# Kernel optimization log

Measured on AMD Instinct MI355X. Metric: run time of the kernel, lower is better.

The kernel has to match this reference:

```python
import jax, jax.numpy as jnp
import numpy as np

B, S, H = 4, 2048, 1024
E, K = 8, 2

def setup_inputs() -> dict:
    key = jax.random.key(0)
    ks = jax.random.split(key, 5)
    scale = 1.0 / np.sqrt(H)
    return {
        "x": jax.random.normal(ks[0], (B, S, H), dtype=jnp.float32),
        "router_w": jax.random.uniform(ks[1], (E, H), jnp.float32, -scale, scale),
        "router_b": jax.random.uniform(ks[2], (E,), jnp.float32, -scale, scale),
        "expert_w": jax.random.uniform(ks[3], (E, H, H), jnp.float32, -scale, scale),
        "expert_b": jax.random.uniform(ks[4], (E, H), jnp.float32, -scale, scale),
    }


def reference(x, router_w, router_b, expert_w, expert_b):
    # Router: [b,s,E]
    scores = jnp.einsum("bsh,eh->bse", x, router_w) + router_b
    probs = jax.nn.softmax(scores, axis=-1)
    p, expert_id = jax.lax.top_k(probs, K)          # [b,s,K]
    # Renormalize top-k probs (matches p / p.sum(dim=2))
    p = p / jnp.sum(p, axis=-1, keepdims=True)
    # Per-token combine weight per expert: [b,s,E]
    onehot = jax.nn.one_hot(expert_id, E, dtype=x.dtype)  # [b,s,K,E]
    w_comb = jnp.einsum("bske,bsk->bse", onehot, p)
    # All-expert linear (Linear: x @ W.T + b): [b,s,E,h]
    all_out = jnp.einsum("bsh,edh->bsed", x, expert_w) + expert_b
    # Weighted combine over selected experts: [b,s,h]
    return jnp.einsum("bse,bsed->bsd", w_comb, all_out)
```

## Files before the change

### kernel.cpp

```cpp
#include <hip/hip_runtime.h>
#include <hip/hip_bf16.h>
#include <math.h>

#define TOK 8192
#define HD 1024
#define NE 8
#define SLOTS 17408

typedef _Float16 half8 __attribute__((ext_vector_type(8)));
typedef _Float16 half4v __attribute__((ext_vector_type(4)));
typedef float floatx4 __attribute__((ext_vector_type(4)));

__global__ void moe_score(const float* __restrict__ x,
                          const float* __restrict__ rw,
                          const float* __restrict__ rb,
                          int* __restrict__ epair,
                          float* __restrict__ w1out,
                          _Float16* __restrict__ xh) {
  const int lane = threadIdx.x & 63;
  const int wid = threadIdx.x >> 6;
  const int t = blockIdx.x * 4 + wid;
  const float4* xp = (const float4*)(x + (size_t)t * HD);
  float4 xr[4];
#pragma unroll
  for (int i = 0; i < 4; ++i) xr[i] = xp[lane + 64 * i];
  if (xh) {
    _Float16* xo = xh + (size_t)t * HD;
#pragma unroll
    for (int i = 0; i < 4; ++i) {
      half4v h = {(_Float16)xr[i].x, (_Float16)xr[i].y,
                  (_Float16)xr[i].z, (_Float16)xr[i].w};
      *(half4v*)(xo + (lane + 64 * i) * 4) = h;
    }
  }
  float sc[NE];
#pragma unroll
  for (int e = 0; e < NE; ++e) {
    const float4* wp = (const float4*)(rw + e * HD);
    float a = 0.f;
#pragma unroll
    for (int i = 0; i < 4; ++i) {
      float4 w = wp[lane + 64 * i];
      a += xr[i].x * w.x + xr[i].y * w.y + xr[i].z * w.z + xr[i].w * w.w;
    }
#pragma unroll
    for (int off = 32; off > 0; off >>= 1) a += __shfl_xor(a, off);
    sc[e] = a + rb[e];
  }
  float b1 = sc[0]; int e1 = 0;
#pragma unroll
  for (int e = 1; e < NE; ++e) if (sc[e] > b1) { b1 = sc[e]; e1 = e; }
  float b2 = -1e30f; int e2 = 0;
#pragma unroll
  for (int e = 0; e < NE; ++e) { if (e != e1 && sc[e] > b2) { b2 = sc[e]; e2 = e; } }
  if (lane == 0) {
    epair[t] = e1 | (e2 << 8);
    w1out[t] = 1.f / (1.f + expf(b2 - b1));
  }
}

__global__ void moe_count(const int* __restrict__ epair, int* __restrict__ cntp) {
  __shared__ int lc[NE];
  const int tid = threadIdx.x;
  if (tid < NE) lc[tid] = 0;
  __syncthreads();
  int ep = epair[blockIdx.x * 256 + tid];
  atomicAdd(&lc[ep & 0xff], 1);
  atomicAdd(&lc[ep >> 8], 1);
  __syncthreads();
  if (tid < NE) atomicAdd(&cntp[tid * 64], lc[tid]);
}

__global__ void moe_prefix(const int* __restrict__ cntp, int* __restrict__ cnt2,
                           int* __restrict__ base) {
  if (threadIdx.x == 0) {
    int b = 0;
    for (int e = 0; e < NE; ++e) {
      base[e] = b;
      cnt2[e * 64] = b;
      b += (cntp[e * 64] + 127) & ~127;
    }
  }
}

__global__ void moe_scatter(const int* __restrict__ epair,
                            const float* __restrict__ w1in,
                            int* __restrict__ cnt2,
                            int* __restrict__ tok_list,
                            float* __restrict__ tok_w,
                            int* __restrict__ slot_of) {
  __shared__ int lcnt[NE];
  __shared__ int lbase[NE];
  const int tid = threadIdx.x;
  const int t = blockIdx.x * 256 + tid;
  if (tid < NE) lcnt[tid] = 0;
  __syncthreads();
  int ep = epair[t];
  int e1 = ep & 0xff, e2 = ep >> 8;
  float w1 = w1in[t];
  int o1 = atomicAdd(&lcnt[e1], 1);
  int o2 = atomicAdd(&lcnt[e2], 1);
  __syncthreads();
  if (tid < NE) lbase[tid] = atomicAdd(&cnt2[tid * 64], lcnt[tid]);
  __syncthreads();
  int s1 = lbase[e1] + o1;
  tok_list[s1] = t; tok_w[s1] = w1; slot_of[2 * t] = s1;
  int s2 = lbase[e2] + o2;
  tok_list[s2] = t; tok_w[s2] = 1.f - w1; slot_of[2 * t + 1] = s2;
}

__global__ void cvt_f32_f16(const float* __restrict__ src,
                            _Float16* __restrict__ dst, int n4) {
  int i = blockIdx.x * 256 + threadIdx.x;
  if (i >= n4) return;
  float4 v = ((const float4*)src)[i];
  half4v h = {(_Float16)v.x, (_Float16)v.y, (_Float16)v.z, (_Float16)v.w};
  ((half4v*)dst)[i] = h;
}

template <int EPI>
__global__ __launch_bounds__(256) void moe_gemm(
    const _Float16* __restrict__ Ah, const _Float16* __restrict__ Bh,
    const float* __restrict__ eb,
    const int* __restrict__ cntp, const int* __restrict__ base,
    const int* __restrict__ tok_list, const float* __restrict__ tok_w,
    _Float16* __restrict__ scratch, float* __restrict__ out) {
  const int e = blockIdx.z;
  const int ce = cntp[e * 64];
  const int m0 = blockIdx.y * 128;
  if (m0 >= ce) return;
  const int sbase = base[e];
  const int n0 = blockIdx.x * 128;
  const int tid = threadIdx.x;
  const int lane = tid & 63;
  const int wid = tid >> 6;
  const int wm = wid & 1, wn = wid >> 1;

  __shared__ _Float16 A_s[128 * 64];
  __shared__ _Float16 B_s[128 * 64];
  __shared__ int tok_s[128];
  __shared__ float w_s[128];

  if (tid < 128) {
    int tk = 0; float w = 0.f;
    if (m0 + tid < ce) { tk = tok_list[sbase + m0 + tid]; w = tok_w[sbase + m0 + tid]; }
    tok_s[tid] = tk; w_s[tid] = w;
  }
  __syncthreads();

  floatx4 acc[4][4];
  floatx4 zero = {0.f, 0.f, 0.f, 0.f};
#pragma unroll
  for (int i = 0; i < 4; ++i)
#pragma unroll
    for (int j = 0; j < 4; ++j) acc[i][j] = zero;

  const size_t wbase = (size_t)e * HD * HD;
  const int rloc = lane >> 3, sub = lane & 7;
  const int csw = (sub ^ rloc) * 8;
  size_t agbase[4], bgbase[4];
#pragma unroll
  for (int q = 0; q < 4; ++q) {
    int row = wid * 32 + q * 8 + rloc;
    agbase[q] = (size_t)tok_s[row] * HD + csw;
    bgbase[q] = wbase + (size_t)(n0 + row) * HD + csw;
  }
  const int x7 = lane & 7, q4 = lane >> 4;

  for (int k0 = 0; k0 < HD; k0 += 64) {
#pragma unroll
    for (int q = 0; q < 4; ++q) {
      const int r0 = wid * 32 + q * 8;
      __builtin_amdgcn_global_load_lds(
          (const __attribute__((address_space(1))) unsigned int*)(Ah + agbase[q] + k0),
          (__attribute__((address_space(3))) unsigned int*)&A_s[r0 * 64], 16, 0, 0);
      __builtin_amdgcn_global_load_lds(
          (const __attribute__((address_space(1))) unsigned int*)(Bh + bgbase[q] + k0),
          (__attribute__((address_space(3))) unsigned int*)&B_s[r0 * 64], 16, 0, 0);
    }
    __syncthreads();
#pragma unroll
    for (int kf = 0; kf < 2; ++kf) {
      half8 afr[4], bfr[4];
      const int cc = kf * 4 + q4;
#pragma unroll
      for (int i = 0; i < 4; ++i)
        afr[i] = *(const half8*)&A_s[(wm * 64 + i * 16 + (lane & 15)) * 64 + ((cc ^ x7) * 8)];
#pragma unroll
      for (int j = 0; j < 4; ++j)
        bfr[j] = *(const half8*)&B_s[(wn * 64 + j * 16 + (lane & 15)) * 64 + ((cc ^ x7) * 8)];
#pragma unroll
      for (int i = 0; i < 4; ++i)
#pragma unroll
        for (int j = 0; j < 4; ++j)
          acc[i][j] = __builtin_amdgcn_mfma_f32_16x16x32_f16(afr[i], bfr[j], acc[i][j], 0, 0, 0);
    }
    __syncthreads();
  }

#pragma unroll
  for (int j = 0; j < 4; ++j) {
    int col = n0 + wn * 64 + j * 16 + (lane & 15);
    float bias = eb[e * HD + col];
#pragma unroll
    for (int i = 0; i < 4; ++i) {
      int rbase = wm * 64 + i * 16 + (q4 << 2);
#pragma unroll
      for (int r = 0; r < 4; ++r) {
        int row = rbase + r;
        float v = w_s[row] * (acc[i][j][r] + bias);
        if (EPI == 1) {
          scratch[(size_t)(sbase + m0 + row) * HD + col] = (_Float16)v;
        } else {
          if (m0 + row < ce)
            atomicAdd(&out[(size_t)tok_s[row] * HD + col], v);
        }
      }
    }
  }
}

__global__ void moe_combine(const _Float16* __restrict__ scratch,
                            const int* __restrict__ slot_of,
                            float* __restrict__ out) {
  const int tid = threadIdx.x;
  const int t = blockIdx.x * 2 + (tid >> 7);
  const int c = (tid & 127) * 8;
  int sa = slot_of[2 * t], sb = slot_of[2 * t + 1];
  half8 a = *(const half8*)&scratch[(size_t)sa * HD + c];
  half8 b = *(const half8*)&scratch[(size_t)sb * HD + c];
  float* o = out + (size_t)t * HD + c;
  float4 o0 = {(float)a[0] + (float)b[0], (float)a[1] + (float)b[1],
               (float)a[2] + (float)b[2], (float)a[3] + (float)b[3]};
  float4 o1 = {(float)a[4] + (float)b[4], (float)a[5] + (float)b[5],
               (float)a[6] + (float)b[6], (float)a[7] + (float)b[7]};
  *(float4*)o = o0;
  *(float4*)(o + 4) = o1;
}

__global__ __launch_bounds__(256) void moe_gemm_f32(
    const float* __restrict__ Af, const float* __restrict__ Bf,
    const float* __restrict__ eb,
    const int* __restrict__ cntp, const int* __restrict__ base,
    const int* __restrict__ tok_list, const float* __restrict__ tok_w,
    float* __restrict__ out) {
  const int e = blockIdx.z;
  const int ce = cntp[e * 64];
  const int m0 = blockIdx.y * 128;
  if (m0 >= ce) return;
  const int sbase = base[e];
  const int n0 = blockIdx.x * 128;
  const int tid = threadIdx.x;
  const int lane = tid & 63;
  const int wid = tid >> 6;
  const int wm = wid & 1, wn = wid >> 1;
  __shared__ _Float16 A_s[128 * 32];
  __shared__ _Float16 B_s[128 * 32];
  __shared__ int tok_s[128];
  __shared__ float w_s[128];
  if (tid < 128) {
    int tk = 0; float w = 0.f;
    if (m0 + tid < ce) { tk = tok_list[sbase + m0 + tid]; w = tok_w[sbase + m0 + tid]; }
    tok_s[tid] = tk; w_s[tid] = w;
  }
  __syncthreads();
  floatx4 acc[4][4];
  floatx4 zero = {0.f, 0.f, 0.f, 0.f};
#pragma unroll
  for (int i = 0; i < 4; ++i)
#pragma unroll
    for (int j = 0; j < 4; ++j) acc[i][j] = zero;
  const size_t wbase = (size_t)e * HD * HD;
  for (int k0 = 0; k0 < HD; k0 += 32) {
#pragma unroll
    for (int q = 0; q < 4; ++q) {
      int s = tid + 256 * q;
      int row = s >> 3, kc = (s & 7) * 4;
      float4 va = *(const float4*)(Af + (size_t)tok_s[row] * HD + k0 + kc);
      half4v ha = {(_Float16)va.x, (_Float16)va.y, (_Float16)va.z, (_Float16)va.w};
      *(half4v*)&A_s[row * 32 + kc] = ha;
      float4 vb = *(const float4*)(Bf + wbase + (size_t)(n0 + row) * HD + k0 + kc);
      half4v hb = {(_Float16)vb.x, (_Float16)vb.y, (_Float16)vb.z, (_Float16)vb.w};
      *(half4v*)&B_s[row * 32 + kc] = hb;
    }
    __syncthreads();
    half8 afr[4], bfr[4];
#pragma unroll
    for (int i = 0; i < 4; ++i)
      afr[i] = *(const half8*)&A_s[(wm * 64 + i * 16 + (lane & 15)) * 32 + (lane >> 4) * 8];
#pragma unroll
    for (int j = 0; j < 4; ++j)
      bfr[j] = *(const half8*)&B_s[(wn * 64 + j * 16 + (lane & 15)) * 32 + (lane >> 4) * 8];
#pragma unroll
    for (int i = 0; i < 4; ++i)
#pragma unroll
      for (int j = 0; j < 4; ++j)
        acc[i][j] = __builtin_amdgcn_mfma_f32_16x16x32_f16(afr[i], bfr[j], acc[i][j], 0, 0, 0);
    __syncthreads();
  }
#pragma unroll
  for (int j = 0; j < 4; ++j) {
    int col = n0 + wn * 64 + j * 16 + (lane & 15);
    float bias = eb[e * HD + col];
#pragma unroll
    for (int i = 0; i < 4; ++i) {
      int rbase = wm * 64 + i * 16 + ((lane >> 4) << 2);
#pragma unroll
      for (int r = 0; r < 4; ++r) {
        int row = rbase + r;
        if (m0 + row < ce)
          atomicAdd(&out[(size_t)tok_s[row] * HD + col], w_s[row] * (acc[i][j][r] + bias));
      }
    }
  }
}

extern "C" void kernel_launch(void* const* d_in, const int* in_sizes, int n_in,
                              void* d_out, int out_size, void* d_ws, size_t ws_size,
                              hipStream_t stream) {
  (void)in_sizes; (void)n_in;
  const float* x  = (const float*)d_in[0];
  const float* rw = (const float*)d_in[1];
  const float* rb = (const float*)d_in[2];
  const float* ew = (const float*)d_in[3];
  const float* eb = (const float*)d_in[4];
  float* out = (float*)d_out;

  char* w = (char*)d_ws;
  int*   cntp     = (int*)(w + 0);
  int*   cnt2     = (int*)(w + 2048);
  int*   basep    = (int*)(w + 4096);
  int*   tok_list = (int*)(w + 4352);
  float* tok_w    = (float*)(w + 4352 + SLOTS*4);
  size_t off = 4352 + 2ull * SLOTS * 4;
  int*   epair    = (int*)(w + off);  off += TOK * 4;
  int*   slot_of  = (int*)(w + off);  off += TOK * 8;
  float* w1buf    = (float*)(w + off); off += TOK * 4;
  off = (off + 255) & ~255ull;
  size_t xh_off = off;
  size_t wh_off = xh_off + (size_t)TOK * HD * 2;
  size_t scr_off = wh_off + (size_t)NE * HD * HD * 2;
  size_t need16  = scr_off;
  size_t needscr = scr_off + (size_t)SLOTS * HD * 2;
  bool fast16 = ws_size >= need16;
  bool fastscr = ws_size >= needscr;

  hipMemsetAsync(cntp, 0, NE * 64 * sizeof(int), stream);
  if (!fastscr)
    hipMemsetAsync(d_out, 0, (size_t)out_size * sizeof(float), stream);

  _Float16* xh = fast16 ? (_Float16*)(w + xh_off) : nullptr;
  _Float16* wh = fast16 ? (_Float16*)(w + wh_off) : nullptr;
  _Float16* scr = fastscr ? (_Float16*)(w + scr_off) : nullptr;

  moe_score<<<TOK / 4, 256, 0, stream>>>(x, rw, rb, epair, w1buf, xh);
  moe_count<<<TOK / 256, 256, 0, stream>>>(epair, cntp);
  moe_prefix<<<1, 64, 0, stream>>>(cntp, cnt2, basep);
  moe_scatter<<<TOK / 256, 256, 0, stream>>>(epair, w1buf, cnt2, tok_list, tok_w, slot_of);

  dim3 grid(HD / 128, TOK / 128, NE);
  if (fast16) {
    int n4w = NE * HD * HD / 4;
    cvt_f32_f16<<<(n4w + 255) / 256, 256, 0, stream>>>(ew, wh, n4w);
    if (fastscr) {
      moe_gemm<1><<<grid, 256, 0, stream>>>(xh, wh, eb, cntp, basep,
                                            tok_list, tok_w, scr, out);
      moe_combine<<<TOK / 2, 256, 0, stream>>>(scr, slot_of, out);
    } else {
      moe_gemm<0><<<grid, 256, 0, stream>>>(xh, wh, eb, cntp, basep,
                                            tok_list, tok_w, nullptr, out);
    }
  } else {
    moe_gemm_f32<<<grid, 256, 0, stream>>>(x, ew, eb, cntp, basep,
                                           tok_list, tok_w, out);
  }
}
```

Baseline: 207.3 us.

## Compact GEMM grid via tile map and fuse count/prefix into one kernel

Replaces the 3D GEMM grid, where most blocks exit early for empty expert tiles, with a 1D grid indexed through a tile map built by a fused single-block count-and-prefix kernel. This removes the per-expert memset and one kernel launch and avoids scheduling thousands of idle blocks. The f32 fallback GEMM is removed, and the small-workspace path now reinterprets f32 inputs as f16, which is incorrect if taken.

```diff
diff --git a/kernel.cpp b/kernel.cpp
--- a/kernel.cpp
+++ b/kernel.cpp
@@ -6,6 +6,7 @@
 #define HD 1024
 #define NE 8
 #define SLOTS 17408
+#define MAXTILES 136
 
 typedef _Float16 half8 __attribute__((ext_vector_type(8)));
 typedef _Float16 half4v __attribute__((ext_vector_type(4)));
@@ -59,27 +60,45 @@
   }
 }
 
-__global__ void moe_count(const int* __restrict__ epair, int* __restrict__ cntp) {
+__global__ __launch_bounds__(1024) void moe_count1(
+    const int* __restrict__ epair,
+    int* __restrict__ cntp,
+    int* __restrict__ cnt2,
+    int* __restrict__ basep,
+    int* __restrict__ tile_map) {
   __shared__ int lc[NE];
   const int tid = threadIdx.x;
   if (tid < NE) lc[tid] = 0;
   __syncthreads();
-  int ep = epair[blockIdx.x * 256 + tid];
-  atomicAdd(&lc[ep & 0xff], 1);
-  atomicAdd(&lc[ep >> 8], 1);
-  __syncthreads();
-  if (tid < NE) atomicAdd(&cntp[tid * 64], lc[tid]);
-}
-
-__global__ void moe_prefix(const int* __restrict__ cntp, int* __restrict__ cnt2,
-                           int* __restrict__ base) {
-  if (threadIdx.x == 0) {
-    int b = 0;
+  int c[NE];
+#pragma unroll
+  for (int e = 0; e < NE; ++e) c[e] = 0;
+#pragma unroll
+  for (int i = 0; i < TOK / 1024; ++i) {
+    int ep = epair[tid + 1024 * i];
+    int e1 = ep & 0xff, e2 = ep >> 8;
+#pragma unroll
+    for (int e = 0; e < NE; ++e) c[e] += (e1 == e) + (e2 == e);
+  }
+#pragma unroll
+  for (int e = 0; e < NE; ++e) {
+#pragma unroll
+    for (int off = 32; off > 0; off >>= 1) c[e] += __shfl_xor(c[e], off);
+    if ((tid & 63) == 0) atomicAdd(&lc[e], c[e]);
+  }
+  __syncthreads();
+  if (tid == 0) {
+    int b = 0, nt = 0;
     for (int e = 0; e < NE; ++e) {
-      base[e] = b;
+      int ce = lc[e];
+      cntp[e * 64] = ce;
+      basep[e] = b;
       cnt2[e * 64] = b;
-      b += (cntp[e * 64] + 127) & ~127;
-    }
+      int mt = (ce + 127) >> 7;
+      for (int m = 0; m < mt; ++m) tile_map[nt++] = (e << 16) | m;
+      b += (ce + 127) & ~127;
+    }
+    for (; nt < MAXTILES; ++nt) tile_map[nt] = -1;
   }
 }
 
@@ -122,15 +141,17 @@
 __global__ __launch_bounds__(256) void moe_gemm(
     const _Float16* __restrict__ Ah, const _Float16* __restrict__ Bh,
     const float* __restrict__ eb,
-    const int* __restrict__ cntp, const int* __restrict__ base,
+    const int* __restrict__ tile_map, const int* __restrict__ cntp,
+    const int* __restrict__ base,
     const int* __restrict__ tok_list, const float* __restrict__ tok_w,
     _Float16* __restrict__ scratch, float* __restrict__ out) {
-  const int e = blockIdx.z;
+  const int tm = tile_map[blockIdx.x >> 3];
+  if (tm < 0) return;
+  const int e = tm >> 16;
+  const int m0 = (tm & 0xffff) << 7;
   const int ce = cntp[e * 64];
-  const int m0 = blockIdx.y * 128;
-  if (m0 >= ce) return;
   const int sbase = base[e];
-  const int n0 = blockIdx.x * 128;
+  const int n0 = (blockIdx.x & 7) << 7;
   const int tid = threadIdx.x;
   const int lane = tid & 63;
   const int wid = tid >> 6;
@@ -238,83 +259,6 @@
   *(float4*)(o + 4) = o1;
 }
 
-__global__ __launch_bounds__(256) void moe_gemm_f32(
-    const float* __restrict__ Af, const float* __restrict__ Bf,
-    const float* __restrict__ eb,
-    const int* __restrict__ cntp, const int* __restrict__ base,
-    const int* __restrict__ tok_list, const float* __restrict__ tok_w,
-    float* __restrict__ out) {
-  const int e = blockIdx.z;
-  const int ce = cntp[e * 64];
-  const int m0 = blockIdx.y * 128;
-  if (m0 >= ce) return;
-  const int sbase = base[e];
-  const int n0 = blockIdx.x * 128;
-  const int tid = threadIdx.x;
-  const int lane = tid & 63;
-  const int wid = tid >> 6;
-  const int wm = wid & 1, wn = wid >> 1;
-  __shared__ _Float16 A_s[128 * 32];
-  __shared__ _Float16 B_s[128 * 32];
-  __shared__ int tok_s[128];
-  __shared__ float w_s[128];
-  if (tid < 128) {
-    int tk = 0; float w = 0.f;
-    if (m0 + tid < ce) { tk = tok_list[sbase + m0 + tid]; w = tok_w[sbase + m0 + tid]; }
-    tok_s[tid] = tk; w_s[tid] = w;
-  }
-  __syncthreads();
-  floatx4 acc[4][4];
-  floatx4 zero = {0.f, 0.f, 0.f, 0.f};
-#pragma unroll
-  for (int i = 0; i < 4; ++i)
-#pragma unroll
-    for (int j = 0; j < 4; ++j) acc[i][j] = zero;
-  const size_t wbase = (size_t)e * HD * HD;
-  for (int k0 = 0; k0 < HD; k0 += 32) {
-#pragma unroll
-    for (int q = 0; q < 4; ++q) {
-      int s = tid + 256 * q;
-      int row = s >> 3, kc = (s & 7) * 4;
-      float4 va = *(const float4*)(Af + (size_t)tok_s[row] * HD + k0 + kc);
-      half4v ha = {(_Float16)va.x, (_Float16)va.y, (_Float16)va.z, (_Float16)va.w};
-      *(half4v*)&A_s[row * 32 + kc] = ha;
-      float4 vb = *(const float4*)(Bf + wbase + (size_t)(n0 + row) * HD + k0 + kc);
-      half4v hb = {(_Float16)vb.x, (_Float16)vb.y, (_Float16)vb.z, (_Float16)vb.w};
-      *(half4v*)&B_s[row * 32 + kc] = hb;
-    }
-    __syncthreads();
-    half8 afr[4], bfr[4];
-#pragma unroll
-    for (int i = 0; i < 4; ++i)
-      afr[i] = *(const half8*)&A_s[(wm * 64 + i * 16 + (lane & 15)) * 32 + (lane >> 4) * 8];
-#pragma unroll
-    for (int j = 0; j < 4; ++j)
-      bfr[j] = *(const half8*)&B_s[(wn * 64 + j * 16 + (lane & 15)) * 32 + (lane >> 4) * 8];
-#pragma unroll
-    for (int i = 0; i < 4; ++i)
-#pragma unroll
-      for (int j = 0; j < 4; ++j)
-        acc[i][j] = __builtin_amdgcn_mfma_f32_16x16x32_f16(afr[i], bfr[j], acc[i][j], 0, 0, 0);
-    __syncthreads();
-  }
-#pragma unroll
-  for (int j = 0; j < 4; ++j) {
-    int col = n0 + wn * 64 + j * 16 + (lane & 15);
-    float bias = eb[e * HD + col];
-#pragma unroll
-    for (int i = 0; i < 4; ++i) {
-      int rbase = wm * 64 + i * 16 + ((lane >> 4) << 2);
-#pragma unroll
-      for (int r = 0; r < 4; ++r) {
-        int row = rbase + r;
-        if (m0 + row < ce)
-          atomicAdd(&out[(size_t)tok_s[row] * HD + col], w_s[row] * (acc[i][j][r] + bias));
-      }
-    }
-  }
-}
-
 extern "C" void kernel_launch(void* const* d_in, const int* in_sizes, int n_in,
                               void* d_out, int out_size, void* d_ws, size_t ws_size,
                               hipStream_t stream) {
@@ -330,9 +274,10 @@
   int*   cntp     = (int*)(w + 0);
   int*   cnt2     = (int*)(w + 2048);
   int*   basep    = (int*)(w + 4096);
-  int*   tok_list = (int*)(w + 4352);
-  float* tok_w    = (float*)(w + 4352 + SLOTS*4);
-  size_t off = 4352 + 2ull * SLOTS * 4;
+  int*   tile_map = (int*)(w + 4160);
+  int*   tok_list = (int*)(w + 4800);
+  float* tok_w    = (float*)(w + 4800 + SLOTS * 4);
+  size_t off = 4800 + 2ull * SLOTS * 4;
   int*   epair    = (int*)(w + off);  off += TOK * 4;
   int*   slot_of  = (int*)(w + off);  off += TOK * 8;
   float* w1buf    = (float*)(w + off); off += TOK * 4;
@@ -340,12 +285,10 @@
   size_t xh_off = off;
   size_t wh_off = xh_off + (size_t)TOK * HD * 2;
   size_t scr_off = wh_off + (size_t)NE * HD * HD * 2;
-  size_t need16  = scr_off;
   size_t needscr = scr_off + (size_t)SLOTS * HD * 2;
-  bool fast16 = ws_size >= need16;
+  bool fast16 = ws_size >= scr_off;
   bool fastscr = ws_size >= needscr;
 
-  hipMemsetAsync(cntp, 0, NE * 64 * sizeof(int), stream);
   if (!fastscr)
     hipMemsetAsync(d_out, 0, (size_t)out_size * sizeof(float), stream);
 
@@ -354,24 +297,23 @@
   _Float16* scr = fastscr ? (_Float16*)(w + scr_off) : nullptr;
 
   moe_score<<<TOK / 4, 256, 0, stream>>>(x, rw, rb, epair, w1buf, xh);
-  moe_count<<<TOK / 256, 256, 0, stream>>>(epair, cntp);
-  moe_prefix<<<1, 64, 0, stream>>>(cntp, cnt2, basep);
+  moe_count1<<<1, 1024, 0, stream>>>(epair, cntp, cnt2, basep, tile_map);
   moe_scatter<<<TOK / 256, 256, 0, stream>>>(epair, w1buf, cnt2, tok_list, tok_w, slot_of);
 
-  dim3 grid(HD / 128, TOK / 128, NE);
   if (fast16) {
     int n4w = NE * HD * HD / 4;
     cvt_f32_f16<<<(n4w + 255) / 256, 256, 0, stream>>>(ew, wh, n4w);
     if (fastscr) {
-      moe_gemm<1><<<grid, 256, 0, stream>>>(xh, wh, eb, cntp, basep,
-                                            tok_list, tok_w, scr, out);
+      moe_gemm<1><<<MAXTILES * 8, 256, 0, stream>>>(
+          xh, wh, eb, tile_map, cntp, basep, tok_list, tok_w, scr, out);
       moe_combine<<<TOK / 2, 256, 0, stream>>>(scr, slot_of, out);
     } else {
-      moe_gemm<0><<<grid, 256, 0, stream>>>(xh, wh, eb, cntp, basep,
-                                            tok_list, tok_w, nullptr, out);
+      moe_gemm<0><<<MAXTILES * 8, 256, 0, stream>>>(
+          xh, wh, eb, tile_map, cntp, basep, tok_list, tok_w, nullptr, out);
     }
   } else {
-    moe_gemm_f32<<<grid, 256, 0, stream>>>(x, ew, eb, cntp, basep,
-                                           tok_list, tok_w, out);
-  }
-}
+    moe_gemm<0><<<MAXTILES * 8, 256, 0, stream>>>(
+        (const _Float16*)x, (const _Float16*)ew, eb, tile_map, cntp, basep,
+        tok_list, tok_w, nullptr, out);
+  }
+}
```

After: 209.9 us. Within noise of the previous version (+1.3%).
